# Performance work log

Hardware: AMD Instinct MI355X
Metric: run time of the kernel (lower is better)

## Reference

```python
import jax, jax.numpy as jnp
import numpy as np

MAX_HOPS = 3


def setup_inputs() -> dict:
    key = jax.random.key(0)
    ks = jax.random.split(key, 6)
    B, M, S = 128, 200, 20
    V, D = 100000, 128
    NC, CL = 10000, 10
    stories = jax.random.randint(ks[0], (B, M, S), 0, V, dtype=jnp.int64)
    queries = jax.random.randint(ks[1], (B, S), 0, V, dtype=jnp.int64)
    candidates = jax.random.randint(ks[2], (NC, CL), 0, V, dtype=jnp.int64)
    # 0.05 scale keeps hop softmax logits in a sane range
    A_tab = jax.random.normal(ks[3], (V, D), dtype=jnp.float32) * 0.05
    W_tab = jax.random.normal(ks[4], (V, D), dtype=jnp.float32) * 0.05
    H_w = jax.random.normal(ks[5], (D, D), dtype=jnp.float32) * 0.05
    return {"stories": stories, "queries": queries, "candidates": candidates,
            "A_tab": A_tab, "W_tab": W_tab, "H_w": H_w}


def reference(stories, queries, candidates, A_tab, W_tab, H_w):
    # padding_idx=0: embedding row 0 is zero
    A = A_tab.at[0].set(0.0)
    W = W_tab.at[0].set(0.0)
    # query encoding: gather + sum-pool -> [B, D]
    u = jnp.sum(A[queries], axis=1)
    # memory encoding: [B, M, D] (same A table each hop, as in the source)
    m = jnp.sum(A[stories], axis=2)
    for _ in range(MAX_HOPS):
        dotted = jnp.einsum('bmd,bd->bm', m, u)          # attention logits
        probs = jax.nn.softmax(dotted, axis=1)           # [B, M]
        o = jnp.einsum('bm,bmd->bd', probs, m)           # weighted memory sum
        u = jnp.tanh(u @ H_w.T + o)                      # Linear(no bias) + tanh
    cand_sum = jnp.sum(W[candidates], axis=1)            # [NC, D]
    logits = u @ cand_sum.T                              # [B, NC]
    return logits
```

## Files before the change

### kernel.cpp

```cpp
#include <hip/hip_runtime.h>
#include <hip/hip_bf16.h>
#include <math.h>

#define BB 128
#define MM 200
#define SS 20
#define DD 128
#define NC 10000
#define CL 10
#define LCT 64

__device__ __forceinline__ unsigned pack_bf16(float a, float b) {
    unsigned ua = __float_as_uint(a), ub = __float_as_uint(b);
    ua += 0x7fff + ((ua >> 16) & 1);
    ub += 0x7fff + ((ub >> 16) & 1);
    return (ua >> 16) | (ub & 0xffff0000u);
}
__device__ __forceinline__ float bflo(unsigned v) { return __uint_as_float(v << 16); }
__device__ __forceinline__ float bfhi(unsigned v) { return __uint_as_float(v & 0xffff0000u); }

__device__ __forceinline__ int detect_shift(const int* __restrict__ q) {
    int zc = 0;
#pragma unroll
    for (int i = 0; i < 8; ++i) zc += (q[2 * i + 1] == 0);
    return (zc >= 6) ? 1 : 0;
}

__global__ __launch_bounds__(512) void k_conv(const float* __restrict__ A,
                                              unsigned* __restrict__ Abf) {
    size_t t = (size_t)blockIdx.x * 512 + threadIdx.x;
    const float4* in = (const float4*)(A + t * 8);
    float4 a = in[0], b = in[1];
    if (t * 8 < DD) {
        a = make_float4(0.f, 0.f, 0.f, 0.f);
        b = make_float4(0.f, 0.f, 0.f, 0.f);
    }
    uint4 o;
    o.x = pack_bf16(a.x, a.y);
    o.y = pack_bf16(a.z, a.w);
    o.z = pack_bf16(b.x, b.y);
    o.w = pack_bf16(b.z, b.w);
    ((uint4*)(Abf + t * 4))[0] = o;
}

__global__ __launch_bounds__(512) void k_main(const int* __restrict__ stories,
                                              const int* __restrict__ queries,
                                              const int* __restrict__ cands,
                                              const unsigned* __restrict__ Abf,
                                              const float* __restrict__ W,
                                              const float* __restrict__ Hw,
                                              float* __restrict__ uT,
                                              float* __restrict__ cand_buf) {
    __shared__ unsigned m_s[MM][DD / 2];
    __shared__ float u_s[DD];
    __shared__ float p_s[MM];
    __shared__ float o_part[8][DD];
    __shared__ float red_s;

    int bid = blockIdx.x;
    int tid = threadIdx.x;
    int shift = detect_shift(queries);

    if (bid < BB) {
        int b = bid;
        int g = tid >> 4, l = tid & 15;
#pragma unroll
        for (int r = 0; r < 7; ++r) {
            int mm = g + (r << 5);
            if (mm < MM) {
                int toks[SS];
#pragma unroll
                for (int s = 0; s < SS; ++s)
                    toks[s] = stories[((size_t)((b * MM + mm) * SS + s)) << shift];
                float a[8] = {0.f, 0.f, 0.f, 0.f, 0.f, 0.f, 0.f, 0.f};
#pragma unroll
                for (int s = 0; s < SS; ++s) {
                    uint4 v = ((const uint4*)(Abf + (size_t)toks[s] * (DD / 2)))[l];
                    a[0] += bflo(v.x); a[1] += bfhi(v.x);
                    a[2] += bflo(v.y); a[3] += bfhi(v.y);
                    a[4] += bflo(v.z); a[5] += bfhi(v.z);
                    a[6] += bflo(v.w); a[7] += bfhi(v.w);
                }
                uint4 o;
                o.x = pack_bf16(a[0], a[1]);
                o.y = pack_bf16(a[2], a[3]);
                o.z = pack_bf16(a[4], a[5]);
                o.w = pack_bf16(a[6], a[7]);
                *(uint4*)&m_s[mm][4 * l] = o;
            }
        }
        if (tid < DD) {
            int d = tid;
            float acc = 0.f;
#pragma unroll
            for (int s = 0; s < SS; ++s) {
                int tok = queries[((size_t)(b * SS + s)) << shift];
                unsigned pv = Abf[(size_t)tok * (DD / 2) + (d >> 1)];
                acc += (d & 1) ? bfhi(pv) : bflo(pv);
            }
            u_s[d] = acc;
        }
        __syncthreads();

        for (int hop = 0; hop < 3; ++hop) {
            if (tid < MM) {
                const float2* u2 = (const float2*)u_s;
                float acc = 0.f;
#pragma unroll 8
                for (int li = 0; li < 64; ++li) {
                    int j = (tid + li) & 63;
                    unsigned pv = m_s[tid][j];
                    float2 uv = u2[j];
                    acc += bflo(pv) * uv.x + bfhi(pv) * uv.y;
                }
                p_s[tid] = acc;
            }
            __syncthreads();
            if (tid < 64) {
                float v0 = p_s[tid], v1 = p_s[tid + 64], v2 = p_s[tid + 128];
                float v3 = (tid < 8) ? p_s[tid + 192] : -1e30f;
                float mx = fmaxf(fmaxf(v0, v1), fmaxf(v2, v3));
                for (int off = 32; off; off >>= 1) mx = fmaxf(mx, __shfl_down(mx, off));
                mx = __shfl(mx, 0);
                float e0 = __expf(v0 - mx), e1 = __expf(v1 - mx), e2 = __expf(v2 - mx);
                float e3 = (tid < 8) ? __expf(v3 - mx) : 0.f;
                float sm = e0 + e1 + e2 + e3;
                for (int off = 32; off; off >>= 1) sm += __shfl_down(sm, off);
                p_s[tid] = e0;
                p_s[tid + 64] = e1;
                p_s[tid + 128] = e2;
                if (tid < 8) p_s[tid + 192] = e3;
                if (tid == 0) red_s = 1.f / __shfl(sm, 0);
            }
            __syncthreads();
            {
                int c = tid & 63, h = tid >> 6;
                int mm0 = h * 25;
                float ax = 0.f, ay = 0.f;
#pragma unroll 5
                for (int k = 0; k < 25; ++k) {
                    unsigned pv = m_s[mm0 + k][c];
                    float p = p_s[mm0 + k];
                    ax = fmaf(p, bflo(pv), ax);
                    ay = fmaf(p, bfhi(pv), ay);
                }
                o_part[h][2 * c] = ax;
                o_part[h][2 * c + 1] = ay;
            }
            __syncthreads();
            float u_new = 0.f;
            if (tid < DD) {
                float o = 0.f;
#pragma unroll
                for (int h = 0; h < 8; ++h) o += o_part[h][tid];
                float acc = o * red_s;
                const float4* hrow = (const float4*)(Hw + tid * DD);
                const float4* u4 = (const float4*)u_s;
#pragma unroll 8
                for (int j = 0; j < DD / 4; ++j) {
                    float4 hv = hrow[j];
                    float4 uv = u4[j];
                    acc += hv.x * uv.x + hv.y * uv.y + hv.z * uv.z + hv.w * uv.w;
                }
                u_new = tanhf(acc);
            }
            __syncthreads();
            if (tid < DD) u_s[tid] = u_new;
            __syncthreads();
        }
        if (tid < DD) uT[tid * BB + bid] = u_s[tid];
    } else {
        int g = tid >> 5, l = tid & 31;
        int row = (bid - BB) * 16 + g;
        int toks[CL];
#pragma unroll
        for (int s = 0; s < CL; ++s)
            toks[s] = cands[((size_t)(row * CL + s)) << shift];
        float4 acc = make_float4(0.f, 0.f, 0.f, 0.f);
#pragma unroll
        for (int s = 0; s < CL; ++s) {
            float4 v = ((const float4*)(W + (size_t)toks[s] * DD))[l];
            float msk = toks[s] ? 1.f : 0.f;
            acc.x = fmaf(msk, v.x, acc.x);
            acc.y = fmaf(msk, v.y, acc.y);
            acc.z = fmaf(msk, v.z, acc.z);
            acc.w = fmaf(msk, v.w, acc.w);
        }
        ((float4*)(cand_buf + (size_t)row * DD))[l] = acc;
    }
}

__global__ __launch_bounds__(256) void k_logits(const float* __restrict__ uT,
                                                const float* __restrict__ cs,
                                                float* __restrict__ out) {
    __shared__ float c_s[DD][LCT + 4];
    int c0 = blockIdx.x * LCT;
    int tid = threadIdx.x;
    {
        int c = tid >> 2, l = tid & 3;
        int row = c0 + c;
        if (row >= NC) row = NC - 1;
        const float4* rp = (const float4*)(cs + (size_t)row * DD);
#pragma unroll
        for (int i = 0; i < 8; ++i) {
            int k = (l << 5) + (i << 2);
            float4 v = rp[(l << 3) + i];
            c_s[k][c] = v.x;
            c_s[k + 1][c] = v.y;
            c_s[k + 2][c] = v.z;
            c_s[k + 3][c] = v.w;
        }
    }
    __syncthreads();
    int tx = tid & 31, ty = tid >> 5;
    const float* cb = &c_s[0][ty << 3];
    const float4* up = (const float4*)(uT + (tx << 2));
    float acc[4][8];
#pragma unroll
    for (int i = 0; i < 4; ++i)
#pragma unroll
        for (int j = 0; j < 8; ++j) acc[i][j] = 0.f;
#pragma unroll 4
    for (int k = 0; k < DD; ++k) {
        float4 uv = up[k * (BB / 4)];
        float4 ca = *(const float4*)(cb + k * (LCT + 4));
        float4 cc = *(const float4*)(cb + k * (LCT + 4) + 4);
        float uu[4] = {uv.x, uv.y, uv.z, uv.w};
        float cv[8] = {ca.x, ca.y, ca.z, ca.w, cc.x, cc.y, cc.z, cc.w};
#pragma unroll
        for (int i = 0; i < 4; ++i)
#pragma unroll
            for (int j = 0; j < 8; ++j) acc[i][j] = fmaf(uu[i], cv[j], acc[i][j]);
    }
    if (c0 + (ty << 3) < NC) {
#pragma unroll
        for (int i = 0; i < 4; ++i) {
            float* orow = out + (size_t)((tx << 2) + i) * NC + c0 + (ty << 3);
            ((float4*)orow)[0] = make_float4(acc[i][0], acc[i][1], acc[i][2], acc[i][3]);
            ((float4*)orow)[1] = make_float4(acc[i][4], acc[i][5], acc[i][6], acc[i][7]);
        }
    }
}

extern "C" void kernel_launch(void* const* d_in, const int* in_sizes, int n_in,
                              void* d_out, int out_size, void* d_ws, size_t ws_size,
                              hipStream_t stream) {
    const int* stories = (const int*)d_in[0];
    const int* queries = (const int*)d_in[1];
    const int* cands   = (const int*)d_in[2];
    const float* A  = (const float*)d_in[3];
    const float* W  = (const float*)d_in[4];
    const float* Hw = (const float*)d_in[5];
    float* out = (float*)d_out;

    unsigned* Abf = (unsigned*)d_ws;
    float* cand_buf = (float*)(Abf + 100000 * (DD / 2));
    float* uT_buf = cand_buf + (size_t)NC * DD;

    k_conv<<<100000 * DD / 8 / 512, 512, 0, stream>>>(A, Abf);
    k_main<<<BB + NC / 16, 512, 0, stream>>>(stories, queries, cands, Abf, W, Hw,
                                             uT_buf, cand_buf);
    k_logits<<<(NC + LCT - 1) / LCT, 256, 0, stream>>>(uT_buf, cand_buf, out);
}
```

Before: 184.6 us.

## Drop bf16 table conversion and split gather from hop attention kernel

Removes the pass that converted the whole A embedding table to bf16, and gathers fp32 rows directly with zero-token masking. Story, query and candidate gathers now run in one wide 512-block kernel that writes bf16 memory rows to workspace. A separate 128-block kernel then runs the attention hops, reading memory from global instead of shared memory. The aim is to cut the full-table conversion traffic and spread the gather across all CUs, at the cost of an extra launch, a workspace round-trip, and a wave-shuffle reduction per memory row for the logits.

```diff
diff --git a/kernel.cpp b/kernel.cpp
--- a/kernel.cpp
+++ b/kernel.cpp
@@ -1,12 +1,11 @@
 #include <hip/hip_runtime.h>
-#include <hip/hip_bf16.h>
 #include <math.h>
 
 #define BB 128
 #define MM 200
 #define SS 20
 #define DD 128
-#define NC 10000
+#define NCC 10000
 #define CL 10
 #define LCT 64
 
@@ -26,168 +25,165 @@
     return (zc >= 6) ? 1 : 0;
 }
 
-__global__ __launch_bounds__(512) void k_conv(const float* __restrict__ A,
-                                              unsigned* __restrict__ Abf) {
-    size_t t = (size_t)blockIdx.x * 512 + threadIdx.x;
-    const float4* in = (const float4*)(A + t * 8);
-    float4 a = in[0], b = in[1];
-    if (t * 8 < DD) {
-        a = make_float4(0.f, 0.f, 0.f, 0.f);
-        b = make_float4(0.f, 0.f, 0.f, 0.f);
-    }
-    uint4 o;
-    o.x = pack_bf16(a.x, a.y);
-    o.y = pack_bf16(a.z, a.w);
-    o.z = pack_bf16(b.x, b.y);
-    o.w = pack_bf16(b.z, b.w);
-    ((uint4*)(Abf + t * 4))[0] = o;
-}
-
-__global__ __launch_bounds__(512) void k_main(const int* __restrict__ stories,
-                                              const int* __restrict__ queries,
-                                              const int* __restrict__ cands,
-                                              const unsigned* __restrict__ Abf,
-                                              const float* __restrict__ W,
-                                              const float* __restrict__ Hw,
-                                              float* __restrict__ uT,
-                                              float* __restrict__ cand_buf) {
-    __shared__ unsigned m_s[MM][DD / 2];
-    __shared__ float u_s[DD];
-    __shared__ float p_s[MM];
-    __shared__ float o_part[8][DD];
-    __shared__ float red_s;
-
-    int bid = blockIdx.x;
-    int tid = threadIdx.x;
+__global__ __launch_bounds__(512) void k_gather(const int* __restrict__ stories,
+                                                const int* __restrict__ queries,
+                                                const int* __restrict__ cands,
+                                                const float* __restrict__ A,
+                                                const float* __restrict__ W,
+                                                unsigned* __restrict__ m_ws,
+                                                float* __restrict__ cand_ws,
+                                                float* __restrict__ u_ws) {
+    int gid = blockIdx.x, tid = threadIdx.x;
     int shift = detect_shift(queries);
-
-    if (bid < BB) {
-        int b = bid;
-        int g = tid >> 4, l = tid & 15;
-#pragma unroll
-        for (int r = 0; r < 7; ++r) {
-            int mm = g + (r << 5);
-            if (mm < MM) {
-                int toks[SS];
-#pragma unroll
-                for (int s = 0; s < SS; ++s)
-                    toks[s] = stories[((size_t)((b * MM + mm) * SS + s)) << shift];
-                float a[8] = {0.f, 0.f, 0.f, 0.f, 0.f, 0.f, 0.f, 0.f};
-#pragma unroll
-                for (int s = 0; s < SS; ++s) {
-                    uint4 v = ((const uint4*)(Abf + (size_t)toks[s] * (DD / 2)))[l];
-                    a[0] += bflo(v.x); a[1] += bfhi(v.x);
-                    a[2] += bflo(v.y); a[3] += bfhi(v.y);
-                    a[4] += bflo(v.z); a[5] += bfhi(v.z);
-                    a[6] += bflo(v.w); a[7] += bfhi(v.w);
-                }
-                uint4 o;
-                o.x = pack_bf16(a[0], a[1]);
-                o.y = pack_bf16(a[2], a[3]);
-                o.z = pack_bf16(a[4], a[5]);
-                o.w = pack_bf16(a[6], a[7]);
-                *(uint4*)&m_s[mm][4 * l] = o;
-            }
-        }
-        if (tid < DD) {
-            int d = tid;
-            float acc = 0.f;
+    int g = tid >> 5, l = tid & 31;
+
+    int base = gid * 50;
+#pragma unroll
+    for (int r = 0; r < 4; ++r) {
+        int rl = (r << 4) + g;
+        if (rl < 50) {
+            int row = base + rl;
+            int toks[SS];
+#pragma unroll
+            for (int s = 0; s < SS; ++s)
+                toks[s] = stories[((size_t)(row * SS + s)) << shift];
+            float4 acc = make_float4(0.f, 0.f, 0.f, 0.f);
 #pragma unroll
             for (int s = 0; s < SS; ++s) {
-                int tok = queries[((size_t)(b * SS + s)) << shift];
-                unsigned pv = Abf[(size_t)tok * (DD / 2) + (d >> 1)];
-                acc += (d & 1) ? bfhi(pv) : bflo(pv);
-            }
-            u_s[d] = acc;
-        }
-        __syncthreads();
-
-        for (int hop = 0; hop < 3; ++hop) {
-            if (tid < MM) {
-                const float2* u2 = (const float2*)u_s;
-                float acc = 0.f;
-#pragma unroll 8
-                for (int li = 0; li < 64; ++li) {
-                    int j = (tid + li) & 63;
-                    unsigned pv = m_s[tid][j];
-                    float2 uv = u2[j];
-                    acc += bflo(pv) * uv.x + bfhi(pv) * uv.y;
-                }
-                p_s[tid] = acc;
-            }
-            __syncthreads();
-            if (tid < 64) {
-                float v0 = p_s[tid], v1 = p_s[tid + 64], v2 = p_s[tid + 128];
-                float v3 = (tid < 8) ? p_s[tid + 192] : -1e30f;
-                float mx = fmaxf(fmaxf(v0, v1), fmaxf(v2, v3));
-                for (int off = 32; off; off >>= 1) mx = fmaxf(mx, __shfl_down(mx, off));
-                mx = __shfl(mx, 0);
-                float e0 = __expf(v0 - mx), e1 = __expf(v1 - mx), e2 = __expf(v2 - mx);
-                float e3 = (tid < 8) ? __expf(v3 - mx) : 0.f;
-                float sm = e0 + e1 + e2 + e3;
-                for (int off = 32; off; off >>= 1) sm += __shfl_down(sm, off);
-                p_s[tid] = e0;
-                p_s[tid + 64] = e1;
-                p_s[tid + 128] = e2;
-                if (tid < 8) p_s[tid + 192] = e3;
-                if (tid == 0) red_s = 1.f / __shfl(sm, 0);
-            }
-            __syncthreads();
-            {
-                int c = tid & 63, h = tid >> 6;
-                int mm0 = h * 25;
-                float ax = 0.f, ay = 0.f;
-#pragma unroll 5
-                for (int k = 0; k < 25; ++k) {
-                    unsigned pv = m_s[mm0 + k][c];
-                    float p = p_s[mm0 + k];
-                    ax = fmaf(p, bflo(pv), ax);
-                    ay = fmaf(p, bfhi(pv), ay);
-                }
-                o_part[h][2 * c] = ax;
-                o_part[h][2 * c + 1] = ay;
-            }
-            __syncthreads();
-            float u_new = 0.f;
-            if (tid < DD) {
-                float o = 0.f;
-#pragma unroll
-                for (int h = 0; h < 8; ++h) o += o_part[h][tid];
-                float acc = o * red_s;
-                const float4* hrow = (const float4*)(Hw + tid * DD);
-                const float4* u4 = (const float4*)u_s;
-#pragma unroll 8
-                for (int j = 0; j < DD / 4; ++j) {
-                    float4 hv = hrow[j];
-                    float4 uv = u4[j];
-                    acc += hv.x * uv.x + hv.y * uv.y + hv.z * uv.z + hv.w * uv.w;
-                }
-                u_new = tanhf(acc);
-            }
-            __syncthreads();
-            if (tid < DD) u_s[tid] = u_new;
-            __syncthreads();
-        }
-        if (tid < DD) uT[tid * BB + bid] = u_s[tid];
-    } else {
-        int g = tid >> 5, l = tid & 31;
-        int row = (bid - BB) * 16 + g;
-        int toks[CL];
-#pragma unroll
-        for (int s = 0; s < CL; ++s)
-            toks[s] = cands[((size_t)(row * CL + s)) << shift];
+                float4 v = ((const float4*)(A + (size_t)toks[s] * DD))[l];
+                float msk = toks[s] ? 1.f : 0.f;
+                acc.x = fmaf(msk, v.x, acc.x);
+                acc.y = fmaf(msk, v.y, acc.y);
+                acc.z = fmaf(msk, v.z, acc.z);
+                acc.w = fmaf(msk, v.w, acc.w);
+            }
+            uint2 o;
+            o.x = pack_bf16(acc.x, acc.y);
+            o.y = pack_bf16(acc.z, acc.w);
+            ((uint2*)(m_ws + (size_t)row * (DD / 2)))[l] = o;
+        }
+    }
+#pragma unroll
+    for (int r = 0; r < 2; ++r) {
+        int rl = (r << 4) + g;
+        int row = gid * 20 + rl;
+        if (rl < 20 && row < NCC) {
+            int toks[CL];
+#pragma unroll
+            for (int s = 0; s < CL; ++s)
+                toks[s] = cands[((size_t)(row * CL + s)) << shift];
+            float4 acc = make_float4(0.f, 0.f, 0.f, 0.f);
+#pragma unroll
+            for (int s = 0; s < CL; ++s) {
+                float4 v = ((const float4*)(W + (size_t)toks[s] * DD))[l];
+                float msk = toks[s] ? 1.f : 0.f;
+                acc.x = fmaf(msk, v.x, acc.x);
+                acc.y = fmaf(msk, v.y, acc.y);
+                acc.z = fmaf(msk, v.z, acc.z);
+                acc.w = fmaf(msk, v.w, acc.w);
+            }
+            ((float4*)(cand_ws + (size_t)row * DD))[l] = acc;
+        }
+    }
+    if (gid < BB && tid < 32) {
+        int toks[SS];
+#pragma unroll
+        for (int s = 0; s < SS; ++s)
+            toks[s] = queries[((size_t)(gid * SS + s)) << shift];
         float4 acc = make_float4(0.f, 0.f, 0.f, 0.f);
 #pragma unroll
-        for (int s = 0; s < CL; ++s) {
-            float4 v = ((const float4*)(W + (size_t)toks[s] * DD))[l];
+        for (int s = 0; s < SS; ++s) {
+            float4 v = ((const float4*)(A + (size_t)toks[s] * DD))[tid];
             float msk = toks[s] ? 1.f : 0.f;
             acc.x = fmaf(msk, v.x, acc.x);
             acc.y = fmaf(msk, v.y, acc.y);
             acc.z = fmaf(msk, v.z, acc.z);
             acc.w = fmaf(msk, v.w, acc.w);
         }
-        ((float4*)(cand_buf + (size_t)row * DD))[l] = acc;
-    }
+        ((float4*)(u_ws + (size_t)gid * DD))[tid] = acc;
+    }
+}
+
+__global__ __launch_bounds__(512) void k_hops(const unsigned* __restrict__ m_ws,
+                                              const float* __restrict__ u_ws,
+                                              const float* __restrict__ Hw,
+                                              float* __restrict__ uT) {
+    __shared__ float u_s[DD];
+    __shared__ float p_s[MM];
+    __shared__ float o_part[8][DD];
+    __shared__ float red_s;
+    int b = blockIdx.x, tid = threadIdx.x;
+    int wave = tid >> 6, lane = tid & 63;
+    const unsigned* mb = m_ws + (size_t)b * MM * (DD / 2);
+
+    if (tid < DD) u_s[tid] = u_ws[b * DD + tid];
+    __syncthreads();
+
+    for (int hop = 0; hop < 3; ++hop) {
+        {
+            float2 uu = ((const float2*)u_s)[lane];
+            for (int i = 0; i < 25; ++i) {
+                int mm = wave * 25 + i;
+                unsigned pv = mb[mm * (DD / 2) + lane];
+                float d = bflo(pv) * uu.x + bfhi(pv) * uu.y;
+                for (int off = 32; off; off >>= 1) d += __shfl_down(d, off);
+                if (lane == 0) p_s[mm] = d;
+            }
+        }
+        __syncthreads();
+        if (tid < 64) {
+            float v0 = p_s[tid], v1 = p_s[tid + 64], v2 = p_s[tid + 128];
+            float v3 = (tid < 8) ? p_s[tid + 192] : -1e30f;
+            float mx = fmaxf(fmaxf(v0, v1), fmaxf(v2, v3));
+            for (int off = 32; off; off >>= 1) mx = fmaxf(mx, __shfl_down(mx, off));
+            mx = __shfl(mx, 0);
+            float e0 = __expf(v0 - mx), e1 = __expf(v1 - mx), e2 = __expf(v2 - mx);
+            float e3 = (tid < 8) ? __expf(v3 - mx) : 0.f;
+            float sm = e0 + e1 + e2 + e3;
+            for (int off = 32; off; off >>= 1) sm += __shfl_down(sm, off);
+            p_s[tid] = e0;
+            p_s[tid + 64] = e1;
+            p_s[tid + 128] = e2;
+            if (tid < 8) p_s[tid + 192] = e3;
+            if (tid == 0) red_s = 1.f / __shfl(sm, 0);
+        }
+        __syncthreads();
+        {
+            int c = tid & 63, h = tid >> 6;
+            int mm0 = h * 25;
+            float ax = 0.f, ay = 0.f;
+#pragma unroll 5
+            for (int k = 0; k < 25; ++k) {
+                unsigned pv = mb[(mm0 + k) * (DD / 2) + c];
+                float p = p_s[mm0 + k];
+                ax = fmaf(p, bflo(pv), ax);
+                ay = fmaf(p, bfhi(pv), ay);
+            }
+            o_part[h][2 * c] = ax;
+            o_part[h][2 * c + 1] = ay;
+        }
+        __syncthreads();
+        float u_new = 0.f;
+        if (tid < DD) {
+            float o = 0.f;
+#pragma unroll
+            for (int h = 0; h < 8; ++h) o += o_part[h][tid];
+            float acc = o * red_s;
+            const float4* hrow = (const float4*)(Hw + tid * DD);
+            const float4* u4 = (const float4*)u_s;
+#pragma unroll 8
+            for (int j = 0; j < DD / 4; ++j) {
+                float4 hv = hrow[j];
+                float4 uv = u4[j];
+                acc += hv.x * uv.x + hv.y * uv.y + hv.z * uv.z + hv.w * uv.w;
+            }
+            u_new = tanhf(acc);
+        }
+        __syncthreads();
+        if (tid < DD) u_s[tid] = u_new;
+        __syncthreads();
+    }
+    if (tid < DD) uT[tid * BB + b] = u_s[tid];
 }
 
 __global__ __launch_bounds__(256) void k_logits(const float* __restrict__ uT,
@@ -199,7 +195,7 @@
     {
         int c = tid >> 2, l = tid & 3;
         int row = c0 + c;
-        if (row >= NC) row = NC - 1;
+        if (row >= NCC) row = NCC - 1;
         const float4* rp = (const float4*)(cs + (size_t)row * DD);
 #pragma unroll
         for (int i = 0; i < 8; ++i) {
@@ -232,10 +228,10 @@
 #pragma unroll
             for (int j = 0; j < 8; ++j) acc[i][j] = fmaf(uu[i], cv[j], acc[i][j]);
     }
-    if (c0 + (ty << 3) < NC) {
+    if (c0 + (ty << 3) < NCC) {
 #pragma unroll
         for (int i = 0; i < 4; ++i) {
-            float* orow = out + (size_t)((tx << 2) + i) * NC + c0 + (ty << 3);
+            float* orow = out + (size_t)((tx << 2) + i) * NCC + c0 + (ty << 3);
             ((float4*)orow)[0] = make_float4(acc[i][0], acc[i][1], acc[i][2], acc[i][3]);
             ((float4*)orow)[1] = make_float4(acc[i][4], acc[i][5], acc[i][6], acc[i][7]);
         }
@@ -253,12 +249,13 @@
     const float* Hw = (const float*)d_in[5];
     float* out = (float*)d_out;
 
-    unsigned* Abf = (unsigned*)d_ws;
-    float* cand_buf = (float*)(Abf + 100000 * (DD / 2));
-    float* uT_buf = cand_buf + (size_t)NC * DD;
-
-    k_conv<<<100000 * DD / 8 / 512, 512, 0, stream>>>(A, Abf);
-    k_main<<<BB + NC / 16, 512, 0, stream>>>(stories, queries, cands, Abf, W, Hw,
-                                             uT_buf, cand_buf);
-    k_logits<<<(NC + LCT - 1) / LCT, 256, 0, stream>>>(uT_buf, cand_buf, out);
-}
+    unsigned* m_ws = (unsigned*)d_ws;
+    float* cand_ws = (float*)(m_ws + (size_t)BB * MM * (DD / 2));
+    float* u_ws = cand_ws + (size_t)NCC * DD;
+    float* uT = u_ws + BB * DD;
+
+    k_gather<<<512, 512, 0, stream>>>(stories, queries, cands, A, W,
+                                      m_ws, cand_ws, u_ws);
+    k_hops<<<BB, 512, 0, stream>>>(m_ws, u_ws, Hw, uT);
+    k_logits<<<(NCC + LCT - 1) / LCT, 256, 0, stream>>>(uT, cand_ws, out);
+}
```

New measurement: 205.6 us. 11.4% more time.
